# Kernel tuning notes

Hardware: AMD Instinct MI355X
Metric: run time of the kernel (lower is better)

The kernel has to match this reference:

```python
import jax, jax.numpy as jnp
import numpy as np

N = 50000          # nodes
E = 640000         # edges (before self-loops)
DIM_FEATS = 128
DIM_H = 32
HEADS1 = 8
NUM_CLASS = 16
NEG_SLOPE_ATT = 0.2   # PyG GATv2Conv default negative_slope
NEG_SLOPE_OUT = 0.01  # F.leaky_relu default


def setup_inputs() -> dict:
    key = jax.random.key(0)
    ks = jax.random.split(key, 12)
    s = 0.1
    x = jax.random.normal(ks[0], (N, DIM_FEATS), dtype=jnp.float32)
    edge_index = jax.random.randint(ks[1], (2, E), 0, N, dtype=jnp.int32)
    # GATv2Conv layer 1: dim_feats -> dim_h per head, 8 heads, concat
    W1l = jax.random.normal(ks[2], (DIM_FEATS, HEADS1 * DIM_H), dtype=jnp.float32) * s
    W1r = jax.random.normal(ks[3], (DIM_FEATS, HEADS1 * DIM_H), dtype=jnp.float32) * s
    att1 = jax.random.normal(ks[4], (HEADS1, DIM_H), dtype=jnp.float32) * s
    b1 = jnp.zeros((HEADS1 * DIM_H,), dtype=jnp.float32)
    # GATv2Conv layer 2: 256 -> num_class, 1 head, concat=False
    W2l = jax.random.normal(ks[5], (HEADS1 * DIM_H, NUM_CLASS), dtype=jnp.float32) * s
    W2r = jax.random.normal(ks[6], (HEADS1 * DIM_H, NUM_CLASS), dtype=jnp.float32) * s
    att2 = jax.random.normal(ks[7], (1, NUM_CLASS), dtype=jnp.float32) * s
    b2 = jnp.zeros((NUM_CLASS,), dtype=jnp.float32)
    return {"x": x, "edge_index": edge_index, "W1l": W1l, "W1r": W1r,
            "att1": att1, "b1": b1, "W2l": W2l, "W2r": W2r,
            "att2": att2, "b2": b2}


def _segment_softmax(scores, seg, num_segments):
    # scores: [E, H], seg: [E] destination node ids
    m = jax.ops.segment_max(scores, seg, num_segments=num_segments)  # [N, H]
    e = jnp.exp(scores - m[seg])
    denom = jax.ops.segment_sum(e, seg, num_segments=num_segments)   # [N, H]
    return e / (denom[seg] + 1e-16)


def _gatv2_layer(x, src, dst, Wl, Wr, att, bias, heads, out_ch, concat):
    n = x.shape[0]
    xl = (x @ Wl).reshape(n, heads, out_ch)  # source transform
    xr = (x @ Wr).reshape(n, heads, out_ch)  # target transform
    # per-edge GATv2 score: a^T LeakyReLU(xl[j] + xr[i])
    e = jax.nn.leaky_relu(xl[src] + xr[dst], negative_slope=NEG_SLOPE_ATT)  # [E,H,F]
    alpha = jnp.einsum('ehf,hf->eh', e, att)                                # [E,H]
    alpha = _segment_softmax(alpha, dst, n)
    msg = xl[src] * alpha[:, :, None]                                       # [E,H,F]
    out = jax.ops.segment_sum(msg, dst, num_segments=n)                     # [N,H,F]
    out = out.reshape(n, heads * out_ch) if concat else out.mean(axis=1)
    return out + bias


def reference(x, edge_index, W1l, W1r, att1, b1, W2l, W2r, att2, b2):
    # add_self_loops=True (PyG GATv2Conv default)
    loop = jnp.arange(N, dtype=edge_index.dtype)
    src = jnp.concatenate([edge_index[0], loop])
    dst = jnp.concatenate([edge_index[1], loop])
    # eval mode: all dropouts are identity
    h = _gatv2_layer(x, src, dst, W1l, W1r, att1, b1, HEADS1, DIM_H, concat=True)
    h = jax.nn.elu(h)
    h = _gatv2_layer(h, src, dst, W2l, W2r, att2, b2, 1, NUM_CLASS, concat=False)
    return jax.nn.leaky_relu(h, negative_slope=NEG_SLOPE_OUT)
```

## Files before the change

kernel.cpp:

```cpp
#include <hip/hip_runtime.h>
#include <math.h>

#define NN 50000
#define E0 640000
#define ET 690000
#define F1 128
#define D1 256
#define C2 16
#define NB 196
#define MPAD 50048
#define PADK 136
#define LOG2E 1.4426950408889634f
#define NBK1 782

typedef _Float16 f16x8 __attribute__((ext_vector_type(8)));
typedef _Float16 h2 __attribute__((ext_vector_type(2)));
typedef __attribute__((ext_vector_type(4))) float f32x4;

__device__ __forceinline__ unsigned short f2h(float f) {
  union { _Float16 h; unsigned short u; } c;
  c.h = (_Float16)f;
  return c.u;
}
__device__ __forceinline__ float h2f(unsigned short u) {
  union { unsigned short u; _Float16 h; } c; c.u = u; return (float)c.h;
}
__device__ __forceinline__ h2 u2h2(unsigned u) {
  union { unsigned u; h2 h; } c; c.u = u; return c.h;
}
__device__ __forceinline__ unsigned h22u(h2 h) {
  union { h2 h; unsigned u; } c; c.h = h; return c.u;
}

template <int CTRL>
__device__ __forceinline__ float dpp_add(float c) {
  int t = __builtin_amdgcn_update_dpp(0, __builtin_bit_cast(int, c), CTRL, 0xF, 0xF, true);
  return c + __builtin_bit_cast(float, t);
}
template <int K>
__device__ __forceinline__ int dpp_bcast(int v) {
  constexpr int ctrl = K | (K << 2) | (K << 4) | (K << 6);
  return __builtin_amdgcn_update_dpp(0, v, ctrl, 0xF, 0xF, true);
}

__global__ __launch_bounds__(256) void k_prep(
    const float* __restrict__ Wl, const float* __restrict__ Wr,
    const float* __restrict__ W2l, const float* __restrict__ W2r,
    const int* __restrict__ ei,
    unsigned short* __restrict__ wt, unsigned short* __restrict__ wt2,
    int* __restrict__ deg) {
  const int b = blockIdx.x;
  if (b < 256) {
    int tid = b * 256 + threadIdx.x;
    int n = tid >> 7, k = tid & 127;
    float v = (n < 256) ? Wl[k * 256 + n] : Wr[k * 256 + (n - 256)];
    wt[tid] = f2h(v);
  } else if (b < 288) {
    int tid = (b - 256) * 256 + threadIdx.x;
    int n = tid >> 8, k = tid & 255;
    float v = (n < 16) ? W2l[k * 16 + n] : W2r[k * 16 + (n - 16)];
    wt2[tid] = f2h(v);
  } else {
    int e = (b - 288) * 256 + threadIdx.x;
    if (e >= ET) return;
    int d = (e < E0) ? ei[E0 + e] : (e - E0);
    atomicAdd(&deg[d], 1);
  }
}

__global__ __launch_bounds__(256) void k_gemm1m(
    const float* __restrict__ x, const unsigned short* __restrict__ wt,
    unsigned short* __restrict__ xlh, unsigned short* __restrict__ xrh) {
  __shared__ unsigned short Al[64 * PADK];
  __shared__ unsigned short Bl[128 * PADK];
  const int t = threadIdx.x;
  const int m0 = blockIdx.x * 64;
  {
    const int r = t >> 4;
    const int c = (t & 15) * 8;
#pragma unroll
    for (int p = 0; p < 4; ++p) {
      const int row = r + p * 16;
      const int rg = m0 + row;
      const float* xp = &x[(size_t)(rg < NN ? rg : NN - 1) * F1 + c];
      float4 lo = *(const float4*)xp;
      float4 hi = *(const float4*)(xp + 4);
      h2 q0 = h2{(_Float16)lo.x, (_Float16)lo.y};
      h2 q1 = h2{(_Float16)lo.z, (_Float16)lo.w};
      h2 q2 = h2{(_Float16)hi.x, (_Float16)hi.y};
      h2 q3 = h2{(_Float16)hi.z, (_Float16)hi.w};
      uint4 st; st.x = h22u(q0); st.y = h22u(q1); st.z = h22u(q2); st.w = h22u(q3);
      *(uint4*)&Al[row * PADK + c] = st;
    }
  }
  const int wave = t >> 6, lane = t & 63;
  const int mw = (wave >> 1) * 32, nw = (wave & 1) * 64;
  const int fr = lane & 15, fq = lane >> 4;
  for (int ny = 0; ny < 4; ++ny) {
    const int n0 = ny * 128;
    {
      const int r = t >> 4;
      const int c = (t & 15) * 8;
#pragma unroll
      for (int p = 0; p < 8; ++p) {
        const int row = r + p * 16;
        *(float4*)&Bl[row * PADK + c] = *(const float4*)&wt[(size_t)(n0 + row) * F1 + c];
      }
    }
    __syncthreads();
    f32x4 acc[2][4] = {};
#pragma unroll
    for (int ks = 0; ks < 4; ++ks) {
      const int ko = ks * 32 + fq * 8;
      f16x8 a[2], b[4];
#pragma unroll
      for (int i = 0; i < 2; ++i)
        a[i] = *(const f16x8*)&Al[(mw + i * 16 + fr) * PADK + ko];
#pragma unroll
      for (int j = 0; j < 4; ++j)
        b[j] = *(const f16x8*)&Bl[(nw + j * 16 + fr) * PADK + ko];
#pragma unroll
      for (int i = 0; i < 2; ++i)
#pragma unroll
        for (int j = 0; j < 4; ++j)
          acc[i][j] = __builtin_amdgcn_mfma_f32_16x16x32_f16(a[i], b[j], acc[i][j], 0, 0, 0);
    }
    __syncthreads();
    unsigned short* outp = (n0 < 256) ? xlh : xrh;
    const int cb = (n0 & 255) + nw + fr;
#pragma unroll
    for (int j = 0; j < 4; ++j) {
      const int col = cb + j * 16;
      const int head = col >> 5, f = col & 31;
      unsigned short* hp = outp + (size_t)head * NN * 32 + f;
#pragma unroll
      for (int i = 0; i < 2; ++i) {
        const int gm0 = m0 + mw + i * 16 + fq * 4;
#pragma unroll
        for (int r = 0; r < 4; ++r) {
          const int gm = gm0 + r;
          if (gm < NN) hp[(size_t)gm * 32] = f2h(acc[i][j][r]);
        }
      }
    }
  }
}

__global__ __launch_bounds__(256) void k_scan_part(const int* __restrict__ deg,
                                                   int* __restrict__ part) {
  int i = blockIdx.x * 256 + threadIdx.x;
  int v = (i < NN) ? deg[i] : 0;
  v += __shfl_xor(v, 1);  v += __shfl_xor(v, 2);  v += __shfl_xor(v, 4);
  v += __shfl_xor(v, 8);  v += __shfl_xor(v, 16); v += __shfl_xor(v, 32);
  __shared__ int w[4];
  if ((threadIdx.x & 63) == 0) w[threadIdx.x >> 6] = v;
  __syncthreads();
  if (threadIdx.x == 0) part[blockIdx.x] = w[0] + w[1] + w[2] + w[3];
}

__global__ __launch_bounds__(256) void k_scan_apply(int* __restrict__ deg,
                                                    const int* __restrict__ part,
                                                    int* __restrict__ offs,
                                                    int* __restrict__ perm) {
  __shared__ int lds[256];
  __shared__ int red[4];
  __shared__ int bh[64];
  __shared__ int bb[64];
  const int b = blockIdx.x, t = threadIdx.x;
  const int i = b * 256 + t;
  int v = (i < NN) ? deg[i] : 0;
  lds[t] = v;
  if (t < 64) bh[t] = 0;
  int pp = 0;
  for (int j = t; j < b; j += 256) pp += part[j];
  pp += __shfl_xor(pp, 1);  pp += __shfl_xor(pp, 2);  pp += __shfl_xor(pp, 4);
  pp += __shfl_xor(pp, 8);  pp += __shfl_xor(pp, 16); pp += __shfl_xor(pp, 32);
  if ((t & 63) == 0) red[t >> 6] = pp;
  __syncthreads();
  int bkt = 0, lpos = 0;
  if (i < NN) {
    bkt = 63 - (v < 63 ? v : 63);
    lpos = atomicAdd(&bh[bkt], 1);
  }
  const int prefix = red[0] + red[1] + red[2] + red[3];
  for (int off = 1; off < 256; off <<= 1) {
    int u = (t >= off) ? lds[t - off] : 0;
    __syncthreads();
    lds[t] += u;
    __syncthreads();
  }
  int excl = prefix + lds[t] - v;
  if (i < NN) { offs[i] = excl; deg[i] = excl; }
  if (b == NB - 1 && t == 255) offs[NN] = prefix + lds[255];
  if (t < 64) {
    int x = bh[t];
    int s = x;
    for (int off = 1; off < 64; off <<= 1) {
      int u = __shfl_up(s, off);
      if (t >= off) s += u;
    }
    bb[t] = s - x;
  }
  __syncthreads();
  if (i < NN) perm[b * 256 + bb[bkt] + lpos] = i;
}

__global__ void k_scatter(const int* __restrict__ ei, int* __restrict__ cur,
                          unsigned short* __restrict__ csr) {
  int e = blockIdx.x * 256 + threadIdx.x;
  if (e >= ET) return;
  int s, d;
  if (e < E0) { s = ei[e]; d = ei[E0 + e]; } else { s = d = e - E0; }
  int pos = atomicAdd(&cur[d], 1);
  csr[pos] = (unsigned short)s;
}

__global__ __launch_bounds__(256) void k_agg1(
    const unsigned short* __restrict__ xlh, const unsigned short* __restrict__ xrh,
    unsigned short* __restrict__ hb,
    const int* __restrict__ offs, const unsigned short* __restrict__ csr,
    const float* __restrict__ att, const float* __restrict__ b1,
    const int* __restrict__ perm) {
  const int b = blockIdx.x;
  const int head = b & 7;
  const int wave = threadIdx.x >> 6;
  const int lane = threadIdx.x & 63;
  const int g = lane >> 2;
  const int j4 = lane & 3;
  const int idxn = (b >> 3) * 64 + wave * 16 + g;
  const bool valid = idxn < NN;
  const int n = valid ? perm[idxn] : 0;
  const int colh = j4 * 8;
  const int col = head * 32 + colh;
  const unsigned short* xlhead = xlh + (size_t)head * NN * 32;

  const uint4 xru = *(const uint4*)&xrh[((size_t)head * NN + n) * 32 + colh];
  h2 xr2[4];
  xr2[0] = u2h2(xru.x); xr2[1] = u2h2(xru.y);
  xr2[2] = u2h2(xru.z); xr2[3] = u2h2(xru.w);
  float at8[8];
  *(float4*)&at8[0] = *(const float4*)&att[col];
  *(float4*)&at8[4] = *(const float4*)&att[col + 4];
  h2 ath6[4], ath4[4];
#pragma unroll
  for (int j = 0; j < 4; ++j) {
    ath6[j] = h2{(_Float16)(at8[2 * j] * (0.6f * LOG2E)),
                 (_Float16)(at8[2 * j + 1] * (0.6f * LOG2E))};
    ath4[j] = h2{(_Float16)(at8[2 * j] * (0.4f * LOG2E)),
                 (_Float16)(at8[2 * j + 1] * (0.4f * LOG2E))};
  }
  float l = 0.f;
  h2 acc2[4] = {h2{0, 0}, h2{0, 0}, h2{0, 0}, h2{0, 0}};
  const int beg = valid ? offs[n] : 0;
  const int fin = valid ? offs[n + 1] : 0;

  auto ldids = [&](int base) -> int {
    int a = base + j4;
    a = (a < fin) ? a : beg;
    return (int)csr[a];
  };
  auto XLrow = [&](int s) -> uint4 {
    return *(const uint4*)&xlhead[(size_t)s * 32 + colh];
  };
  auto edge = [&](const uint4& w, bool live) {
    h2 xh[4];
    xh[0] = u2h2(w.x); xh[1] = u2h2(w.y); xh[2] = u2h2(w.z); xh[3] = u2h2(w.w);
    float cv = 0.f, ca = 0.f;
#pragma unroll
    for (int j = 0; j < 4; ++j) {
      h2 v = xh[j] + xr2[j];
      h2 a = u2h2(h22u(v) & 0x7FFF7FFFu);
      cv = __builtin_amdgcn_fdot2(v, ath6[j], cv, false);
      ca = __builtin_amdgcn_fdot2(a, ath4[j], ca, false);
    }
    float c = cv + ca;
    c = dpp_add<0xB1>(c);
    c = dpp_add<0x4E>(c);
    float p = exp2f(c);
    p = live ? p : 0.f;
    l += p;
    const _Float16 ph = (_Float16)p;
    const h2 p2 = h2{ph, ph};
#pragma unroll
    for (int j = 0; j < 4; ++j) acc2[j] += p2 * xh[j];
  };

  int ids = ldids(beg);
  uint4 w0 = XLrow(dpp_bcast<0>(ids));
  uint4 w1 = XLrow(dpp_bcast<1>(ids));
  uint4 w2 = XLrow(dpp_bcast<2>(ids));
  uint4 w3 = XLrow(dpp_bcast<3>(ids));
  int ids1 = ldids(beg + 4);
  for (int idx = beg; idx < fin; idx += 4) {
    const uint4 v0 = XLrow(dpp_bcast<0>(ids1));
    const uint4 v1 = XLrow(dpp_bcast<1>(ids1));
    const uint4 v2 = XLrow(dpp_bcast<2>(ids1));
    const uint4 v3 = XLrow(dpp_bcast<3>(ids1));
    const int ids2 = ldids(idx + 8);
    edge(w0, true);
    edge(w1, idx + 1 < fin);
    edge(w2, idx + 2 < fin);
    edge(w3, idx + 3 < fin);
    w0 = v0; w1 = v1; w2 = v2; w3 = v3; ids1 = ids2;
  }

  if (valid) {
    const float rl = __builtin_amdgcn_rcpf(l + 1e-16f);
    float b8[8], o[8];
    *(float4*)&b8[0] = *(const float4*)&b1[col];
    *(float4*)&b8[4] = *(const float4*)&b1[col + 4];
#pragma unroll
    for (int j = 0; j < 4; ++j) {
      o[2 * j]     = (float)acc2[j][0] * rl + b8[2 * j];
      o[2 * j + 1] = (float)acc2[j][1] * rl + b8[2 * j + 1];
    }
#pragma unroll
    for (int k = 0; k < 8; ++k)
      o[k] = o[k] > 0.f ? o[k] : exp2f(o[k] * LOG2E) - 1.f;
    ushort4 p;
    p.x = f2h(o[0]); p.y = f2h(o[1]); p.z = f2h(o[2]); p.w = f2h(o[3]);
    ushort4 q;
    q.x = f2h(o[4]); q.y = f2h(o[5]); q.z = f2h(o[6]); q.w = f2h(o[7]);
    uint4 packed;
    packed.x = *(unsigned*)&p.x; packed.y = *(unsigned*)&p.z;
    packed.z = *(unsigned*)&q.x; packed.w = *(unsigned*)&q.z;
    *(uint4*)&hb[(size_t)n * D1 + col] = packed;
  }
}

__global__ __launch_bounds__(256) void k_gemm2m(
    const unsigned short* __restrict__ hb, const unsigned short* __restrict__ wt2,
    unsigned short* __restrict__ h2lh, float* __restrict__ h2r) {
  const int t = threadIdx.x;
  const int wave = t >> 6, lane = t & 63;
  const int fr = lane & 15, fq = lane >> 4;
  const int m0 = blockIdx.x * 128 + wave * 32;
  f32x4 acc[2][2] = {};
#pragma unroll
  for (int ks = 0; ks < 8; ++ks) {
    const int ko = ks * 32 + fq * 8;
    f16x8 a[2], b[2];
#pragma unroll
    for (int i = 0; i < 2; ++i) {
      int row = m0 + i * 16 + fr; if (row >= NN) row = NN - 1;
      a[i] = *(const f16x8*)&hb[(size_t)row * D1 + ko];
    }
#pragma unroll
    for (int j = 0; j < 2; ++j)
      b[j] = *(const f16x8*)&wt2[(j * 16 + fr) * 256 + ko];
#pragma unroll
    for (int i = 0; i < 2; ++i)
#pragma unroll
      for (int j = 0; j < 2; ++j)
        acc[i][j] = __builtin_amdgcn_mfma_f32_16x16x32_f16(a[i], b[j], acc[i][j], 0, 0, 0);
  }
#pragma unroll
  for (int i = 0; i < 2; ++i) {
    const int gm0 = m0 + i * 16 + fq * 4;
#pragma unroll
    for (int r = 0; r < 4; ++r) {
      const int gm = gm0 + r;
      if (gm < NN) {
        h2lh[(size_t)gm * C2 + fr] = f2h(acc[i][0][r]);
        h2r[(size_t)gm * C2 + fr] = acc[i][1][r];
      }
    }
  }
}

__global__ __launch_bounds__(256) void k_agg2(
    const unsigned short* __restrict__ h2lh, const float* __restrict__ h2r,
    const int* __restrict__ offs, const unsigned short* __restrict__ csr,
    const float* __restrict__ att2, const float* __restrict__ b2,
    float* __restrict__ out) {
  const int wave = threadIdx.x >> 6;
  const int lane = threadIdx.x & 63;
  const int n = blockIdx.x * 4 + wave;
  if (n >= NN) return;
  const int c = lane & 15, g = lane >> 4;
  const float xr_v = h2r[(size_t)n * C2 + c];
  const float att_v = att2[c] * LOG2E;
  float l = 0.f, acc = 0.f;
  const int beg = offs[n], fin = offs[n + 1];
  for (int idx = beg + g; idx < fin; idx += 8) {
    const int i1 = idx + 4;
    const bool m1 = i1 < fin;
    const int s0 = csr[idx];
    const int s1 = csr[m1 ? i1 : idx];
    const float xl0 = h2f(h2lh[(size_t)s0 * C2 + c]);
    const float xl1 = h2f(h2lh[(size_t)s1 * C2 + c]);
    float v0 = xl0 + xr_v; v0 = fmaxf(v0, 0.2f * v0);
    float v1 = xl1 + xr_v; v1 = fmaxf(v1, 0.2f * v1);
    float sc0 = v0 * att_v, sc1 = v1 * att_v;
    sc0 = dpp_add<0xB1>(sc0);   sc1 = dpp_add<0xB1>(sc1);
    sc0 = dpp_add<0x4E>(sc0);   sc1 = dpp_add<0x4E>(sc1);
    sc0 = dpp_add<0x124>(sc0);  sc1 = dpp_add<0x124>(sc1);
    sc0 = dpp_add<0x128>(sc0);  sc1 = dpp_add<0x128>(sc1);
    const float p0 = exp2f(sc0);
    const float p1 = m1 ? exp2f(sc1) : 0.f;
    l += p0 + p1;
    acc = fmaf(p0, xl0, fmaf(p1, xl1, acc));
  }
  l += __shfl_xor(l, 16);   l += __shfl_xor(l, 32);
  acc += __shfl_xor(acc, 16); acc += __shfl_xor(acc, 32);
  float o = acc * __builtin_amdgcn_rcpf(l + 1e-16f) + b2[c];
  o = o > 0.f ? o : 0.01f * o;
  if (lane < 16) out[(size_t)n * C2 + c] = o;
}

extern "C" void kernel_launch(void* const* d_in, const int* in_sizes, int n_in,
                              void* d_out, int out_size, void* d_ws, size_t ws_size,
                              hipStream_t stream) {
  const float* x    = (const float*)d_in[0];
  const int*   ei   = (const int*)d_in[1];
  const float* W1l  = (const float*)d_in[2];
  const float* W1r  = (const float*)d_in[3];
  const float* att1 = (const float*)d_in[4];
  const float* b1   = (const float*)d_in[5];
  const float* W2l  = (const float*)d_in[6];
  const float* W2r  = (const float*)d_in[7];
  const float* att2 = (const float*)d_in[8];
  const float* b2   = (const float*)d_in[9];
  float* out = (float*)d_out;

  unsigned short* xlh = (unsigned short*)d_ws;
  unsigned short* xrh = xlh + (size_t)NN * D1;
  unsigned short* hb  = xrh + (size_t)NN * D1;
  int* deg  = (int*)(hb + (size_t)NN * D1);
  int* part = deg + NN;
  int* offs = part + NB;
  int* perm = offs + NN + 1;
  unsigned short* csr = (unsigned short*)(perm + NN);
  unsigned short* wt  = csr + ET + 2;
  unsigned short* wt2 = wt + 512 * F1;
  unsigned short* h2lh = xlh;
  float* h2r = (float*)(h2lh + (size_t)NN * C2);

  hipMemsetAsync(deg, 0, NN * sizeof(int), stream);
  k_prep<<<288 + (ET + 255) / 256, 256, 0, stream>>>(
      W1l, W1r, W2l, W2r, ei, wt, wt2, deg);
  k_gemm1m<<<MPAD / 64, 256, 0, stream>>>(x, wt, xlh, xrh);
  k_scan_part<<<NB, 256, 0, stream>>>(deg, part);
  k_scan_apply<<<NB, 256, 0, stream>>>(deg, part, offs, perm);
  k_scatter<<<(ET + 255) / 256, 256, 0, stream>>>(ei, deg, csr);
  k_agg1<<<NBK1 * 8, 256, 0, stream>>>(xlh, xrh, hb, offs, csr, att1, b1, perm);
  k_gemm2m<<<(NN + 127) / 128, 256, 0, stream>>>(hb, wt2, h2lh, h2r);
  k_agg2<<<NN / 4, 256, 0, stream>>>(h2lh, h2r, offs, csr, att2, b2, out);
}
```

Baseline: 258.1 us.

## Process four nodes per lane group in agg1 with packed node info

```diff
diff --git a/kernel.cpp b/kernel.cpp
--- a/kernel.cpp
+++ b/kernel.cpp
@@ -11,7 +11,7 @@
 #define MPAD 50048
 #define PADK 136
 #define LOG2E 1.4426950408889634f
-#define NBK1 782
+#define NCH 391
 
 typedef _Float16 f16x8 __attribute__((ext_vector_type(8)));
 typedef _Float16 h2 __attribute__((ext_vector_type(2)));
@@ -161,7 +161,8 @@
 __global__ __launch_bounds__(256) void k_scan_apply(int* __restrict__ deg,
                                                     const int* __restrict__ part,
                                                     int* __restrict__ offs,
-                                                    int* __restrict__ perm) {
+                                                    uint2* __restrict__ ninfo,
+                                                    unsigned short* __restrict__ csr) {
   __shared__ int lds[256];
   __shared__ int red[4];
   __shared__ int bh[64];
@@ -190,7 +191,11 @@
     __syncthreads();
   }
   int excl = prefix + lds[t] - v;
-  if (i < NN) { offs[i] = excl; deg[i] = excl; }
+  if (i < NN) {
+    offs[i] = excl;
+    deg[i] = excl + 1;
+    csr[excl] = (unsigned short)i;
+  }
   if (b == NB - 1 && t == 255) offs[NN] = prefix + lds[255];
   if (t < 64) {
     int x = bh[t];
@@ -202,42 +207,37 @@
     bb[t] = s - x;
   }
   __syncthreads();
-  if (i < NN) perm[b * 256 + bb[bkt] + lpos] = i;
+  if (i < NN)
+    ninfo[b * 256 + bb[bkt] + lpos] =
+        make_uint2((unsigned)excl, (unsigned)i | ((unsigned)v << 16));
 }
 
 __global__ void k_scatter(const int* __restrict__ ei, int* __restrict__ cur,
                           unsigned short* __restrict__ csr) {
   int e = blockIdx.x * 256 + threadIdx.x;
-  if (e >= ET) return;
-  int s, d;
-  if (e < E0) { s = ei[e]; d = ei[E0 + e]; } else { s = d = e - E0; }
+  if (e >= E0) return;
+  int s = ei[e], d = ei[E0 + e];
   int pos = atomicAdd(&cur[d], 1);
   csr[pos] = (unsigned short)s;
 }
 
-__global__ __launch_bounds__(256) void k_agg1(
+__global__ __launch_bounds__(128) void k_agg1(
     const unsigned short* __restrict__ xlh, const unsigned short* __restrict__ xrh,
     unsigned short* __restrict__ hb,
-    const int* __restrict__ offs, const unsigned short* __restrict__ csr,
-    const float* __restrict__ att, const float* __restrict__ b1,
-    const int* __restrict__ perm) {
+    const uint2* __restrict__ ninfo, const unsigned short* __restrict__ csr,
+    const float* __restrict__ att, const float* __restrict__ b1) {
   const int b = blockIdx.x;
   const int head = b & 7;
   const int wave = threadIdx.x >> 6;
   const int lane = threadIdx.x & 63;
   const int g = lane >> 2;
   const int j4 = lane & 3;
-  const int idxn = (b >> 3) * 64 + wave * 16 + g;
-  const bool valid = idxn < NN;
-  const int n = valid ? perm[idxn] : 0;
+  const int slot0 = (b >> 3) * 128 + wave * 64 + g;
   const int colh = j4 * 8;
   const int col = head * 32 + colh;
   const unsigned short* xlhead = xlh + (size_t)head * NN * 32;
-
-  const uint4 xru = *(const uint4*)&xrh[((size_t)head * NN + n) * 32 + colh];
-  h2 xr2[4];
-  xr2[0] = u2h2(xru.x); xr2[1] = u2h2(xru.y);
-  xr2[2] = u2h2(xru.z); xr2[3] = u2h2(xru.w);
+  const unsigned short* xrhead = xrh + (size_t)head * NN * 32;
+
   float at8[8];
   *(float4*)&at8[0] = *(const float4*)&att[col];
   *(float4*)&at8[4] = *(const float4*)&att[col + 4];
@@ -249,82 +249,110 @@
     ath4[j] = h2{(_Float16)(at8[2 * j] * (0.4f * LOG2E)),
                  (_Float16)(at8[2 * j + 1] * (0.4f * LOG2E))};
   }
-  float l = 0.f;
-  h2 acc2[4] = {h2{0, 0}, h2{0, 0}, h2{0, 0}, h2{0, 0}};
-  const int beg = valid ? offs[n] : 0;
-  const int fin = valid ? offs[n + 1] : 0;
-
-  auto ldids = [&](int base) -> int {
-    int a = base + j4;
-    a = (a < fin) ? a : beg;
-    return (int)csr[a];
-  };
-  auto XLrow = [&](int s) -> uint4 {
-    return *(const uint4*)&xlhead[(size_t)s * 32 + colh];
-  };
-  auto edge = [&](const uint4& w, bool live) {
-    h2 xh[4];
-    xh[0] = u2h2(w.x); xh[1] = u2h2(w.y); xh[2] = u2h2(w.z); xh[3] = u2h2(w.w);
-    float cv = 0.f, ca = 0.f;
-#pragma unroll
-    for (int j = 0; j < 4; ++j) {
-      h2 v = xh[j] + xr2[j];
-      h2 a = u2h2(h22u(v) & 0x7FFF7FFFu);
-      cv = __builtin_amdgcn_fdot2(v, ath6[j], cv, false);
-      ca = __builtin_amdgcn_fdot2(a, ath4[j], ca, false);
-    }
-    float c = cv + ca;
-    c = dpp_add<0xB1>(c);
-    c = dpp_add<0x4E>(c);
-    float p = exp2f(c);
-    p = live ? p : 0.f;
-    l += p;
-    const _Float16 ph = (_Float16)p;
-    const h2 p2 = h2{ph, ph};
-#pragma unroll
-    for (int j = 0; j < 4; ++j) acc2[j] += p2 * xh[j];
-  };
-
-  int ids = ldids(beg);
-  uint4 w0 = XLrow(dpp_bcast<0>(ids));
-  uint4 w1 = XLrow(dpp_bcast<1>(ids));
-  uint4 w2 = XLrow(dpp_bcast<2>(ids));
-  uint4 w3 = XLrow(dpp_bcast<3>(ids));
-  int ids1 = ldids(beg + 4);
-  for (int idx = beg; idx < fin; idx += 4) {
-    const uint4 v0 = XLrow(dpp_bcast<0>(ids1));
-    const uint4 v1 = XLrow(dpp_bcast<1>(ids1));
-    const uint4 v2 = XLrow(dpp_bcast<2>(ids1));
-    const uint4 v3 = XLrow(dpp_bcast<3>(ids1));
-    const int ids2 = ldids(idx + 8);
-    edge(w0, true);
-    edge(w1, idx + 1 < fin);
-    edge(w2, idx + 2 < fin);
-    edge(w3, idx + 3 < fin);
-    w0 = v0; w1 = v1; w2 = v2; w3 = v3; ids1 = ids2;
-  }
-
-  if (valid) {
-    const float rl = __builtin_amdgcn_rcpf(l + 1e-16f);
-    float b8[8], o[8];
-    *(float4*)&b8[0] = *(const float4*)&b1[col];
-    *(float4*)&b8[4] = *(const float4*)&b1[col + 4];
-#pragma unroll
-    for (int j = 0; j < 4; ++j) {
-      o[2 * j]     = (float)acc2[j][0] * rl + b8[2 * j];
-      o[2 * j + 1] = (float)acc2[j][1] * rl + b8[2 * j + 1];
-    }
-#pragma unroll
-    for (int k = 0; k < 8; ++k)
-      o[k] = o[k] > 0.f ? o[k] : exp2f(o[k] * LOG2E) - 1.f;
-    ushort4 p;
-    p.x = f2h(o[0]); p.y = f2h(o[1]); p.z = f2h(o[2]); p.w = f2h(o[3]);
-    ushort4 q;
-    q.x = f2h(o[4]); q.y = f2h(o[5]); q.z = f2h(o[6]); q.w = f2h(o[7]);
-    uint4 packed;
-    packed.x = *(unsigned*)&p.x; packed.y = *(unsigned*)&p.z;
-    packed.z = *(unsigned*)&q.x; packed.w = *(unsigned*)&q.z;
-    *(uint4*)&hb[(size_t)n * D1 + col] = packed;
+  float b8[8];
+  *(float4*)&b8[0] = *(const float4*)&b1[col];
+  *(float4*)&b8[4] = *(const float4*)&b1[col + 4];
+
+  uint2 info[4];
+#pragma unroll
+  for (int j = 0; j < 4; ++j) {
+    const int s = slot0 + j * 16;
+    info[j] = ninfo[s < NN ? s : NN - 1];
+  }
+  int n_[4], beg_[4], fin_[4], idsA[4], idsB[4];
+  uint4 xru[4];
+#pragma unroll
+  for (int j = 0; j < 4; ++j) {
+    const int s = slot0 + j * 16;
+    const int n = (int)(info[j].y & 0xFFFFu);
+    const int dg = (s < NN) ? (int)(info[j].y >> 16) : 0;
+    const int bg = (int)info[j].x;
+    n_[j] = n; beg_[j] = bg; fin_[j] = bg + dg;
+    xru[j] = *(const uint4*)&xrhead[(size_t)n * 32 + colh];
+    int a0 = bg + j4;     a0 = (a0 < fin_[j]) ? a0 : bg;
+    int a1 = bg + 4 + j4; a1 = (a1 < fin_[j]) ? a1 : bg;
+    idsA[j] = (int)csr[a0];
+    idsB[j] = (int)csr[a1];
+  }
+
+#pragma unroll
+  for (int j = 0; j < 4; ++j) {
+    const int beg = beg_[j], fin = fin_[j], n = n_[j];
+    h2 xr2[4];
+    xr2[0] = u2h2(xru[j].x); xr2[1] = u2h2(xru[j].y);
+    xr2[2] = u2h2(xru[j].z); xr2[3] = u2h2(xru[j].w);
+    float l = 0.f;
+    h2 acc2[4] = {h2{0, 0}, h2{0, 0}, h2{0, 0}, h2{0, 0}};
+
+    auto XLrow = [&](int src) -> uint4 {
+      return *(const uint4*)&xlhead[(size_t)src * 32 + colh];
+    };
+    auto ldids = [&](int base) -> int {
+      int a = base + j4;
+      a = (a < fin) ? a : beg;
+      return (int)csr[a];
+    };
+    auto edge = [&](const uint4& w, bool live) {
+      h2 xh[4];
+      xh[0] = u2h2(w.x); xh[1] = u2h2(w.y); xh[2] = u2h2(w.z); xh[3] = u2h2(w.w);
+      float cv = 0.f, ca = 0.f;
+#pragma unroll
+      for (int q = 0; q < 4; ++q) {
+        h2 v = xh[q] + xr2[q];
+        h2 a = u2h2(h22u(v) & 0x7FFF7FFFu);
+        cv = __builtin_amdgcn_fdot2(v, ath6[q], cv, false);
+        ca = __builtin_amdgcn_fdot2(a, ath4[q], ca, false);
+      }
+      float c = cv + ca;
+      c = dpp_add<0xB1>(c);
+      c = dpp_add<0x4E>(c);
+      float p = exp2f(c);
+      p = live ? p : 0.f;
+      l += p;
+      const _Float16 ph = (_Float16)p;
+      const h2 p2 = h2{ph, ph};
+#pragma unroll
+      for (int q = 0; q < 4; ++q) acc2[q] += p2 * xh[q];
+    };
+
+    int ids = idsA[j];
+    uint4 w0 = XLrow(dpp_bcast<0>(ids));
+    uint4 w1 = XLrow(dpp_bcast<1>(ids));
+    uint4 w2 = XLrow(dpp_bcast<2>(ids));
+    uint4 w3 = XLrow(dpp_bcast<3>(ids));
+    int ids1 = idsB[j];
+    for (int idx = beg; idx < fin; idx += 4) {
+      const uint4 v0 = XLrow(dpp_bcast<0>(ids1));
+      const uint4 v1 = XLrow(dpp_bcast<1>(ids1));
+      const uint4 v2 = XLrow(dpp_bcast<2>(ids1));
+      const uint4 v3 = XLrow(dpp_bcast<3>(ids1));
+      const int ids2 = ldids(idx + 8);
+      edge(w0, true);
+      edge(w1, idx + 1 < fin);
+      edge(w2, idx + 2 < fin);
+      edge(w3, idx + 3 < fin);
+      w0 = v0; w1 = v1; w2 = v2; w3 = v3; ids1 = ids2;
+    }
+
+    if (slot0 + j * 16 < NN) {
+      const float rl = __builtin_amdgcn_rcpf(l + 1e-16f);
+      float o[8];
+#pragma unroll
+      for (int q = 0; q < 4; ++q) {
+        o[2 * q]     = (float)acc2[q][0] * rl + b8[2 * q];
+        o[2 * q + 1] = (float)acc2[q][1] * rl + b8[2 * q + 1];
+      }
+#pragma unroll
+      for (int k = 0; k < 8; ++k)
+        o[k] = o[k] > 0.f ? o[k] : exp2f(o[k] * LOG2E) - 1.f;
+      ushort4 ph, qh;
+      ph.x = f2h(o[0]); ph.y = f2h(o[1]); ph.z = f2h(o[2]); ph.w = f2h(o[3]);
+      qh.x = f2h(o[4]); qh.y = f2h(o[5]); qh.z = f2h(o[6]); qh.w = f2h(o[7]);
+      uint4 packed;
+      packed.x = *(unsigned*)&ph.x; packed.y = *(unsigned*)&ph.z;
+      packed.z = *(unsigned*)&qh.x; packed.w = *(unsigned*)&qh.z;
+      *(uint4*)&hb[(size_t)n * D1 + col] = packed;
+    }
   }
 }
 
@@ -429,8 +457,8 @@
   int* deg  = (int*)(hb + (size_t)NN * D1);
   int* part = deg + NN;
   int* offs = part + NB;
-  int* perm = offs + NN + 1;
-  unsigned short* csr = (unsigned short*)(perm + NN);
+  uint2* ninfo = (uint2*)(offs + NN + 2);
+  unsigned short* csr = (unsigned short*)(ninfo + NN);
   unsigned short* wt  = csr + ET + 2;
   unsigned short* wt2 = wt + 512 * F1;
   unsigned short* h2lh = xlh;
@@ -441,9 +469,9 @@
       W1l, W1r, W2l, W2r, ei, wt, wt2, deg);
   k_gemm1m<<<MPAD / 64, 256, 0, stream>>>(x, wt, xlh, xrh);
   k_scan_part<<<NB, 256, 0, stream>>>(deg, part);
-  k_scan_apply<<<NB, 256, 0, stream>>>(deg, part, offs, perm);
-  k_scatter<<<(ET + 255) / 256, 256, 0, stream>>>(ei, deg, csr);
-  k_agg1<<<NBK1 * 8, 256, 0, stream>>>(xlh, xrh, hb, offs, csr, att1, b1, perm);
+  k_scan_apply<<<NB, 256, 0, stream>>>(deg, part, offs, ninfo, csr);
+  k_scatter<<<(E0 + 255) / 256, 256, 0, stream>>>(ei, deg, csr);
+  k_agg1<<<NCH * 8, 128, 0, stream>>>(xlh, xrh, hb, ninfo, csr, att1, b1);
   k_gemm2m<<<(NN + 127) / 128, 256, 0, stream>>>(hb, wt2, h2lh, h2r);
   k_agg2<<<NN / 4, 256, 0, stream>>>(h2lh, h2r, offs, csr, att2, b2, out);
 }
```

Measured after the change: 264.9 us. +2.6%, slower.
